# Performance work log

Measured on AMD Instinct MI355X. Metric: run time of the kernel, lower is better.

## Reference

```python
import jax, jax.numpy as jnp
import numpy as np

BN_EPS = 1e-5
TEMPERATURE = 256 ** 0.5  # sqrt(c2), since cv3 = ScaledDotProductAttention(c2)


def conv_bn_silu(x, w, gamma, beta, mean, var):
    # Conv2d(k=3, s=1, pad='same', bias=False) -> BatchNorm2d (running stats) -> SiLU
    y = jax.lax.conv_general_dilated(
        x, w, window_strides=(1, 1), padding='SAME',
        dimension_numbers=('NCHW', 'OIHW', 'NCHW'))
    scale = (gamma / jnp.sqrt(var + BN_EPS))[None, :, None, None]
    shift = (beta - mean * gamma / jnp.sqrt(var + BN_EPS))[None, :, None, None]
    y = y * scale + shift
    return y * jax.nn.sigmoid(y)  # SiLU


def setup_inputs() -> dict:
    key = jax.random.key(0)
    ks = jax.random.split(key, 8)
    B, C, H, W = 16, 256, 64, 64
    Ch = 128  # hidden channels c_ = int(c2 * e)
    x = jax.random.normal(ks[0], (B, C, H, W), dtype=jnp.float32)
    w1 = jax.random.normal(ks[1], (Ch, C, 3, 3), dtype=jnp.float32) * 0.05
    g1 = jnp.ones((Ch,), jnp.float32) + 0.1 * jax.random.normal(ks[2], (Ch,), dtype=jnp.float32)
    b1 = 0.1 * jax.random.normal(ks[3], (Ch,), dtype=jnp.float32)
    m1 = 0.1 * jax.random.normal(ks[4], (Ch,), dtype=jnp.float32)
    v1 = jnp.ones((Ch,), jnp.float32) + 0.5 * jax.random.uniform(ks[5], (Ch,), dtype=jnp.float32)
    w2 = jax.random.normal(ks[6], (C, Ch, 3, 3), dtype=jnp.float32) * 0.05
    g2 = jnp.ones((C,), jnp.float32)
    b2 = jnp.zeros((C,), jnp.float32)
    m2 = 0.1 * jax.random.normal(ks[7], (C,), dtype=jnp.float32)
    v2 = jnp.ones((C,), jnp.float32) + 0.5 * jax.random.uniform(jax.random.fold_in(key, 99), (C,), dtype=jnp.float32)
    return {"x": x, "w1": w1, "g1": g1, "b1": b1, "m1": m1, "v1": v1,
            "w2": w2, "g2": g2, "b2": b2, "m2": m2, "v2": v2}


def reference(x, w1, g1, b1, m1, v1, w2, g2, b2, m2, v2):
    y = conv_bn_silu(x, w1, g1, b1, m1, v1)       # [B, 128, H, W]
    y = conv_bn_silu(y, w2, g2, b2, m2, v2)       # [B, 256, H, W]
    B, C, H, W = y.shape
    q = y.reshape(B, C, H * W)                    # q = k^T = v, all views of y
    # channel-channel attention: scores [B, C, C]
    scores = jnp.einsum('bcn,bdn->bcd', q / TEMPERATURE, q)
    attn = jax.nn.softmax(scores, axis=-1)        # dropout is identity in eval
    out = jnp.einsum('bcd,bdn->bcn', attn, q).reshape(B, C, H, W)
    return x + out  # shortcut: c1 == c2
```

## Files before the change

kernel.cpp:

```cpp
#include <hip/hip_runtime.h>
#include <math.h>

#define BB 16
#define C1 256
#define CHD 128
#define NN 4096
#define INV_T (1.0f/16.0f)

typedef _Float16 half8 __attribute__((ext_vector_type(8)));
typedef __attribute__((ext_vector_type(4))) float f32x4;

__device__ inline unsigned short f2h(float f) {
    _Float16 h = (_Float16)f;
    return __builtin_bit_cast(unsigned short, h);
}

#define GLDS(g, l) __builtin_amdgcn_global_load_lds(                              \
    (const __attribute__((address_space(1))) unsigned int*)(g),                   \
    (__attribute__((address_space(3))) unsigned int*)(l), 16, 0, 0)

__global__ __launch_bounds__(256) void nchw_to_nhwc_f16(
    const float* __restrict__ x, unsigned short* __restrict__ xh, int C)
{
    const int c0 = blockIdx.x * 64;
    const int hp = blockIdx.y;
    const int b  = blockIdx.z;

    if (hp == 0 || hp == 65) {
        for (int idx = threadIdx.x; idx < 1024; idx += 256) {
            int w = idx >> 4, cq = (idx & 15) * 4;
            ushort4 z; z.x = z.y = z.z = z.w = 0;
            *(ushort4*)&xh[(((size_t)b * 66 + hp) * 64 + w) * C + c0 + cq] = z;
        }
        return;
    }
    const int h = hp - 1;
    __shared__ float ts[64][65];
    for (int idx = threadIdx.x; idx < 4096; idx += 256) {
        int cl = idx >> 6, w = idx & 63;
        ts[cl][w] = x[(((size_t)b * C + c0 + cl) * 64 + h) * 64 + w];
    }
    __syncthreads();
    for (int idx = threadIdx.x; idx < 1024; idx += 256) {
        int w = idx >> 4, cq = (idx & 15) * 4;
        ushort4 o;
        o.x = f2h(ts[cq + 0][w]); o.y = f2h(ts[cq + 1][w]);
        o.z = f2h(ts[cq + 2][w]); o.w = f2h(ts[cq + 3][w]);
        *(ushort4*)&xh[(((size_t)b * 66 + hp) * 64 + w) * C + c0 + cq] = o;
    }
}

__global__ __launch_bounds__(256) void pack_w_kernel(
    const float* __restrict__ w, unsigned short* __restrict__ wT, int Cout, int Cin)
{
    int idx = blockIdx.x * 256 + threadIdx.x;
    int total = Cout * Cin * 9;
    if (idx >= total) return;
    int ci = idx % Cin; int t = idx / Cin; int co = t % Cout; int kk = t / Cout;
    wT[idx] = f2h(w[((size_t)co * Cin + ci) * 9 + kk]);
}

__global__ __launch_bounds__(256) void zero_y1h_pads(unsigned short* __restrict__ y1h)
{
    int idx = blockIdx.x * 256 + threadIdx.x;
    int b = idx >> 12;
    int row = ((idx >> 11) & 1) ? 65 : 0;
    int inner = idx & 2047;
    ushort4 z; z.x = z.y = z.z = z.w = 0;
    *(ushort4*)&y1h[(((size_t)b * 66 + row) * 64) * 128 + inner * 4] = z;
}

__global__ __launch_bounds__(256) void conv_mfma_kernel(
    const unsigned short* __restrict__ xh, const unsigned short* __restrict__ wT,
    const float* __restrict__ gamma, const float* __restrict__ beta,
    const float* __restrict__ mean, const float* __restrict__ var,
    unsigned short* __restrict__ outNHWC,
    unsigned short* __restrict__ yhi, unsigned short* __restrict__ yhiT,
    int Cin, int Cout)
{
    const int tid  = threadIdx.x;
    const int wid  = tid >> 6;
    const int lane = tid & 63;
    const int ln   = lane & 15;
    const int q    = lane >> 4;
    const int coBase = blockIdx.x * 64;
    const int h0     = blockIdx.y * 4;
    const int b      = blockIdx.z;

    __shared__ unsigned short xs[6 * 66 * 32];
    __shared__ unsigned short ws[9 * 64 * 32];
    __shared__ float bnsc[64], bnsh[64];

    if (tid < 64) {
        int co = coBase + tid;
        float sc = gamma[co] * rsqrtf(var[co] + 1e-5f);
        bnsc[tid] = sc;
        bnsh[tid] = beta[co] - mean[co] * sc;
    }
    if (tid < 48) {
        int r = tid >> 3, cpart = tid & 7;
        int col = (cpart < 4) ? 0 : 65;
        ushort4 z; z.x = z.y = z.z = z.w = 0;
        *(ushort4*)&xs[r * 2112 + col * 32 + (cpart & 3) * 8] = z;
        *(ushort4*)&xs[r * 2112 + col * 32 + (cpart & 3) * 8 + 4] = z;
    }
    __syncthreads();

    f32x4 acc[4][4] = {};

    const int nChunk = Cin >> 5;
    for (int ck = 0; ck < nChunk; ck++) {
        const int ci0 = ck << 5;
        for (int it = wid; it < 60; it += 4) {
            if (it < 36) {
                int el   = it * 512 + lane * 8;
                int kkco = el >> 5;
                int kk   = kkco >> 6;
                int co   = kkco & 63;
                int cip  = el & 31;
                const unsigned short* g =
                    wT + (((size_t)kk * Cout + coBase + co) * Cin + ci0 + cip);
                GLDS(g, ws + it * 512);
            } else {
                int j = it - 36;
                int r = j >> 2, p = j & 3;
                int w   = p * 16 + (lane >> 2);
                int cip = (lane & 3) * 8;
                const unsigned short* g =
                    xh + ((((size_t)b * 66 + h0 + r) * 64 + w) * Cin + ci0 + cip);
                GLDS(g, xs + r * 2112 + (1 + p * 16) * 32);
            }
        }
        __syncthreads();

#pragma unroll
        for (int kk = 0; kk < 9; kk++) {
            const int kh = kk / 3, kw = kk % 3;
            half8 af[4], bfr[4];
#pragma unroll
            for (int mi = 0; mi < 4; mi++)
                af[mi] = *(const half8*)&ws[(kk * 64 + mi * 16 + ln) * 32 + q * 8];
#pragma unroll
            for (int ni = 0; ni < 4; ni++)
                bfr[ni] = *(const half8*)&xs[(wid + kh) * 2112 + (ni * 16 + ln + kw) * 32 + q * 8];
#pragma unroll
            for (int mi = 0; mi < 4; mi++)
#pragma unroll
                for (int ni = 0; ni < 4; ni++)
                    acc[mi][ni] = __builtin_amdgcn_mfma_f32_16x16x32_f16(
                        af[mi], bfr[ni], acc[mi][ni], 0, 0, 0);
        }
        __syncthreads();
    }

    const int orow = h0 + wid;
    if (outNHWC) {
#pragma unroll
        for (int mi = 0; mi < 4; mi++) {
            int col0 = mi * 16 + q * 4;
            float s0 = bnsc[col0 + 0], h0s = bnsh[col0 + 0];
            float s1 = bnsc[col0 + 1], h1s = bnsh[col0 + 1];
            float s2 = bnsc[col0 + 2], h2s = bnsh[col0 + 2];
            float s3 = bnsc[col0 + 3], h3s = bnsh[col0 + 3];
#pragma unroll
            for (int ni = 0; ni < 4; ni++) {
                int w = ni * 16 + ln;
                f32x4 a = acc[mi][ni];
                float t0 = a.x * s0 + h0s, t1 = a.y * s1 + h1s;
                float t2 = a.z * s2 + h2s, t3 = a.w * s3 + h3s;
                ushort4 o;
                o.x = f2h(t0 / (1.f + __expf(-t0)));
                o.y = f2h(t1 / (1.f + __expf(-t1)));
                o.z = f2h(t2 / (1.f + __expf(-t2)));
                o.w = f2h(t3 / (1.f + __expf(-t3)));
                *(ushort4*)&outNHWC[(((size_t)b * 66 + orow + 1) * 64 + w) * Cout
                                    + coBase + col0] = o;
            }
        }
    } else {
#pragma unroll
        for (int mi = 0; mi < 4; mi++) {
            int col0 = mi * 16 + q * 4;
#pragma unroll
            for (int ni = 0; ni < 4; ni++) {
                int w = ni * 16 + ln;
                f32x4 a = acc[mi][ni];
                float vals[4] = {a.x, a.y, a.z, a.w};
                ushort4 hv;
                unsigned short* hvp = (unsigned short*)&hv;
#pragma unroll
                for (int r = 0; r < 4; r++) {
                    int co = coBase + col0 + r;
                    float t = vals[r] * bnsc[col0 + r] + bnsh[col0 + r];
                    float s = t / (1.f + __expf(-t));
                    hvp[r] = f2h(s);
                    yhi[(((size_t)b * Cout + co) * 64 + orow) * 64 + w] = hvp[r];
                }
                *(ushort4*)&yhiT[((size_t)b * 4096 + orow * 64 + w) * Cout
                                 + coBase + col0] = hv;
            }
        }
    }
}

__global__ __launch_bounds__(256) void scores_mfma_kernel(
    const unsigned short* __restrict__ yhi, float* __restrict__ scores)
{
    static const int TI[10] = {0,0,0,0,1,1,1,2,2,3};
    static const int TJ[10] = {0,1,2,3,1,2,3,2,3,3};
    const int b  = blockIdx.z;
    const int ti = TI[blockIdx.x], tj = TJ[blockIdx.x];
    const int cB = ti * 64;
    const int dB = tj * 64;
    const int tid  = threadIdx.x;
    const int wid  = tid >> 6;
    const int lane = tid & 63;
    const int ln   = lane & 15;
    const int q    = lane >> 4;
    const int wm   = wid >> 1, wn = wid & 1;

    __shared__ unsigned short As[64 * 128];
    __shared__ unsigned short Bs[64 * 128];

    const int rl = lane >> 4;
    const int gl = lane & 15;

    f32x4 acc[2][2] = {};

    for (int ck = 0; ck < 32; ck++) {
        const int n0 = ck * 128;
        for (int it = wid; it < 32; it += 4) {
            const int tile = it >> 4;
            const int j = it & 15;
            const int r = j * 4 + rl;
            const int gq = gl ^ (r & 7);
            const int rowAbs = (tile ? dB : cB) + r;
            const unsigned short* g =
                yhi + ((size_t)b * 256 + rowAbs) * 4096 + n0 + gq * 8;
            GLDS(g, (tile ? Bs : As) + j * 512);
        }
        __syncthreads();

#pragma unroll
        for (int kwin = 0; kwin < 4; kwin++) {
            half8 ah[2], bh[2];
#pragma unroll
            for (int mi = 0; mi < 2; mi++) {
                int row = wm * 32 + mi * 16 + ln;
                ah[mi] = *(const half8*)&As[row * 128 + ((kwin * 4 + q) ^ (ln & 7)) * 8];
            }
#pragma unroll
            for (int ni = 0; ni < 2; ni++) {
                int row = wn * 32 + ni * 16 + ln;
                bh[ni] = *(const half8*)&Bs[row * 128 + ((kwin * 4 + q) ^ (ln & 7)) * 8];
            }
#pragma unroll
            for (int mi = 0; mi < 2; mi++)
#pragma unroll
                for (int ni = 0; ni < 2; ni++)
                    acc[mi][ni] = __builtin_amdgcn_mfma_f32_16x16x32_f16(
                        ah[mi], bh[ni], acc[mi][ni], 0, 0, 0);
        }
        __syncthreads();
    }

#pragma unroll
    for (int mi = 0; mi < 2; mi++)
#pragma unroll
        for (int ni = 0; ni < 2; ni++) {
            f32x4 a = acc[mi][ni];
            float vals[4];
            vals[0] = a.x * INV_T; vals[1] = a.y * INV_T;
            vals[2] = a.z * INV_T; vals[3] = a.w * INV_T;
            int c0 = cB + wm * 32 + mi * 16 + q * 4;
            int d  = dB + wn * 32 + ni * 16 + ln;
#pragma unroll
            for (int r = 0; r < 4; r++)
                scores[((size_t)b * C1 + c0 + r) * C1 + d] = vals[r];
            if (ti != tj) {
                float4 tv = {vals[0], vals[1], vals[2], vals[3]};
                *(float4*)&scores[((size_t)b * C1 + d) * C1 + c0] = tv;
            }
        }
}

__global__ __launch_bounds__(64) void softmax_kernel(
    const float* __restrict__ scores, unsigned short* __restrict__ attn16)
{
    const int row = blockIdx.x;
    const float* p = scores + (size_t)row * C1;
    const int lane = threadIdx.x;

    float4 v = ((const float4*)p)[lane];
    float m = fmaxf(fmaxf(v.x, v.y), fmaxf(v.z, v.w));
#pragma unroll
    for (int off = 32; off >= 1; off >>= 1)
        m = fmaxf(m, __shfl_xor(m, off, 64));

    float4 e;
    e.x = expf(v.x - m); e.y = expf(v.y - m);
    e.z = expf(v.z - m); e.w = expf(v.w - m);
    float s = e.x + e.y + e.z + e.w;
#pragma unroll
    for (int off = 32; off >= 1; off >>= 1)
        s += __shfl_xor(s, off, 64);
    float inv = 1.f / s;
    ushort4 o;
    o.x = f2h(e.x * inv); o.y = f2h(e.y * inv);
    o.z = f2h(e.z * inv); o.w = f2h(e.w * inv);
    *(ushort4*)&attn16[(size_t)row * C1 + lane * 4] = o;
}

__global__ __launch_bounds__(256) void out_mfma_kernel(
    const unsigned short* __restrict__ attn16, const unsigned short* __restrict__ yhiT,
    const float* __restrict__ x, float* __restrict__ out)
{
    const int b  = blockIdx.z;
    const int cB = blockIdx.y * 64;
    const int nB = blockIdx.x * 128;
    const int tid  = threadIdx.x;
    const int wid  = tid >> 6;
    const int lane = tid & 63;
    const int ln   = lane & 15;
    const int q    = lane >> 4;
    const int wm   = wid >> 1, wn = wid & 1;

    __shared__ unsigned short As[64 * 64];
    __shared__ unsigned short Bs[128 * 64];

    const int r8 = lane >> 3;
    const int gq = (lane & 7) ^ r8;

    f32x4 acc[2][4] = {};

    for (int ck = 0; ck < 4; ck++) {
        const int d0 = ck * 64;
        for (int it = wid; it < 24; it += 4) {
            if (it < 8) {
                const unsigned short* g =
                    attn16 + ((size_t)b * 256 + cB + it * 8 + r8) * 256 + d0 + gq * 8;
                GLDS(g, As + it * 512);
            } else {
                int j = it - 8;
                const unsigned short* g =
                    yhiT + ((size_t)b * 4096 + nB + j * 8 + r8) * 256 + d0 + gq * 8;
                GLDS(g, Bs + j * 512);
            }
        }
        __syncthreads();

#pragma unroll
        for (int kwin = 0; kwin < 2; kwin++) {
            const int cc = (((kwin * 4 + q) ^ (ln & 7))) * 8;
            half8 af[2], bfr[4];
#pragma unroll
            for (int mi = 0; mi < 2; mi++)
                af[mi] = *(const half8*)&As[(wm * 32 + mi * 16 + ln) * 64 + cc];
#pragma unroll
            for (int ni = 0; ni < 4; ni++)
                bfr[ni] = *(const half8*)&Bs[(wn * 64 + ni * 16 + ln) * 64 + cc];
#pragma unroll
            for (int mi = 0; mi < 2; mi++)
#pragma unroll
                for (int ni = 0; ni < 4; ni++)
                    acc[mi][ni] = __builtin_amdgcn_mfma_f32_16x16x32_f16(
                        af[mi], bfr[ni], acc[mi][ni], 0, 0, 0);
        }
        __syncthreads();
    }

#pragma unroll
    for (int mi = 0; mi < 2; mi++)
#pragma unroll
        for (int ni = 0; ni < 4; ni++) {
            f32x4 a = acc[mi][ni];
            float vals[4] = {a.x, a.y, a.z, a.w};
#pragma unroll
            for (int r = 0; r < 4; r++) {
                int c = cB + wm * 32 + mi * 16 + q * 4 + r;
                int n = nB + wn * 64 + ni * 16 + ln;
                size_t o = ((size_t)b * C1 + c) * NN + n;
                out[o] = x[o] + vals[r];
            }
        }
}

extern "C" void kernel_launch(void* const* d_in, const int* in_sizes, int n_in,
                              void* d_out, int out_size, void* d_ws, size_t ws_size,
                              hipStream_t stream)
{
    const float* x  = (const float*)d_in[0];
    const float* w1 = (const float*)d_in[1];
    const float* g1 = (const float*)d_in[2];
    const float* b1 = (const float*)d_in[3];
    const float* m1 = (const float*)d_in[4];
    const float* v1 = (const float*)d_in[5];
    const float* w2 = (const float*)d_in[6];
    const float* g2 = (const float*)d_in[7];
    const float* b2 = (const float*)d_in[8];
    const float* m2 = (const float*)d_in[9];
    const float* v2 = (const float*)d_in[10];
    float* out = (float*)d_out;

    unsigned short* xh   = (unsigned short*)d_ws;
    unsigned short* y1h  = xh  + (size_t)17301504;
    unsigned short* wt1  = y1h + (size_t)8650752;
    unsigned short* wt2  = wt1 + (size_t)294912;
    unsigned short* yhiT = wt2 + (size_t)294912;
    unsigned short* yhi  = xh;
    float*          sc   = (float*)y1h;
    unsigned short* attn16 = (unsigned short*)(sc + 1048576);

    nchw_to_nhwc_f16<<<dim3(C1 / 64, 66, BB), 256, 0, stream>>>(x, xh, C1);
    pack_w_kernel<<<(9 * CHD * C1 + 255) / 256, 256, 0, stream>>>(w1, wt1, CHD, C1);
    pack_w_kernel<<<(9 * C1 * CHD + 255) / 256, 256, 0, stream>>>(w2, wt2, C1, CHD);
    zero_y1h_pads<<<256, 256, 0, stream>>>(y1h);

    conv_mfma_kernel<<<dim3(CHD / 64, 16, BB), 256, 0, stream>>>(
        xh, wt1, g1, b1, m1, v1, y1h, nullptr, nullptr, C1, CHD);
    conv_mfma_kernel<<<dim3(C1 / 64, 16, BB), 256, 0, stream>>>(
        y1h, wt2, g2, b2, m2, v2, nullptr, yhi, yhiT, CHD, C1);

    scores_mfma_kernel<<<dim3(10, 1, BB), 256, 0, stream>>>(yhi, sc);
    softmax_kernel<<<dim3(BB * C1), 64, 0, stream>>>(sc, attn16);
    out_mfma_kernel<<<dim3(NN / 128, 4, BB), 256, 0, stream>>>(attn16, yhiT, x, out);
}
```

Before: 324.4 us.

## Double-buffer conv LDS staging, switch to 32x32 MFMA, 8-row 512-thread blocks

Restructures the implicit-GEMM convolution kernel so each block covers 8 output rows with 8 waves. The input-channel chunk is cut to 16 and the staging buffers are double-buffered, so the next chunk's global-to-LDS loads are issued while the current chunk is computed. The inner product moves from 16x16x32 to 32x32x16 MFMA, which cuts fragment loads per MFMA, and the epilogue is rewritten to match the new accumulator layout. The costs are smaller chunks and more barriers per chunk, a larger LDS footprint, and a reliance on async LDS loads overlapping without an explicit wait before the barrier.

New measurement: 343.7 us. +6.0%, slower.

```diff
diff --git a/kernel.cpp b/kernel.cpp
--- a/kernel.cpp
+++ b/kernel.cpp
@@ -9,6 +9,7 @@
 
 typedef _Float16 half8 __attribute__((ext_vector_type(8)));
 typedef __attribute__((ext_vector_type(4))) float f32x4;
+typedef __attribute__((ext_vector_type(16))) float f32x16;
 
 __device__ inline unsigned short f2h(float f) {
     _Float16 h = (_Float16)f;
@@ -70,7 +71,7 @@
     *(ushort4*)&y1h[(((size_t)b * 66 + row) * 64) * 128 + inner * 4] = z;
 }
 
-__global__ __launch_bounds__(256) void conv_mfma_kernel(
+__global__ __launch_bounds__(512, 4) void conv_mfma_kernel(
     const unsigned short* __restrict__ xh, const unsigned short* __restrict__ wT,
     const float* __restrict__ gamma, const float* __restrict__ beta,
     const float* __restrict__ mean, const float* __restrict__ var,
@@ -81,14 +82,14 @@
     const int tid  = threadIdx.x;
     const int wid  = tid >> 6;
     const int lane = tid & 63;
-    const int ln   = lane & 15;
-    const int q    = lane >> 4;
+    const int l31  = lane & 31;
+    const int hi   = lane >> 5;
     const int coBase = blockIdx.x * 64;
-    const int h0     = blockIdx.y * 4;
+    const int h0     = blockIdx.y * 8;
     const int b      = blockIdx.z;
 
-    __shared__ unsigned short xs[6 * 66 * 32];
-    __shared__ unsigned short ws[9 * 64 * 32];
+    __shared__ unsigned short xs[2][10560];
+    __shared__ unsigned short ws[2][9216];
     __shared__ float bnsc[64], bnsh[64];
 
     if (tid < 64) {
@@ -97,109 +98,111 @@
         bnsc[tid] = sc;
         bnsh[tid] = beta[co] - mean[co] * sc;
     }
-    if (tid < 48) {
-        int r = tid >> 3, cpart = tid & 7;
-        int col = (cpart < 4) ? 0 : 65;
+    if (tid < 160) {
+        int r    = tid >> 4;
+        int rem  = tid & 15;
+        int buf  = rem >> 3;
+        int rem2 = rem & 7;
+        int col  = (rem2 >> 2) ? 65 : 0;
+        int part = rem2 & 3;
         ushort4 z; z.x = z.y = z.z = z.w = 0;
-        *(ushort4*)&xs[r * 2112 + col * 32 + (cpart & 3) * 8] = z;
-        *(ushort4*)&xs[r * 2112 + col * 32 + (cpart & 3) * 8 + 4] = z;
-    }
+        *(ushort4*)&xs[buf][(r * 66 + col) * 16 + part * 4] = z;
+    }
+
+    auto stage = [&](int sel, int ck) {
+        const int ci0 = ck << 4;
+        for (int it = wid; it < 38; it += 8) {
+            if (it < 18) {
+                int row = it * 32 + (lane >> 1);
+                int kk  = row >> 6;
+                int co  = row & 63;
+                const unsigned short* g =
+                    wT + (((size_t)kk * Cout + coBase + co) * Cin + ci0 + (lane & 1) * 8);
+                GLDS(g, &ws[sel][it * 512]);
+            } else {
+                int j  = it - 18;
+                int r  = j >> 1;
+                int hf = j & 1;
+                int colL = hf * 32 + (lane >> 1);
+                const unsigned short* g =
+                    xh + ((((size_t)b * 66 + h0 + r) * 64 + colL) * Cin + ci0 + (lane & 1) * 8);
+                GLDS(g, &xs[sel][(r * 66 + 1 + hf * 32) * 16]);
+            }
+        }
+    };
+
+    stage(0, 0);
     __syncthreads();
 
-    f32x4 acc[4][4] = {};
-
-    const int nChunk = Cin >> 5;
-    for (int ck = 0; ck < nChunk; ck++) {
-        const int ci0 = ck << 5;
-        for (int it = wid; it < 60; it += 4) {
-            if (it < 36) {
-                int el   = it * 512 + lane * 8;
-                int kkco = el >> 5;
-                int kk   = kkco >> 6;
-                int co   = kkco & 63;
-                int cip  = el & 31;
-                const unsigned short* g =
-                    wT + (((size_t)kk * Cout + coBase + co) * Cin + ci0 + cip);
-                GLDS(g, ws + it * 512);
-            } else {
-                int j = it - 36;
-                int r = j >> 2, p = j & 3;
-                int w   = p * 16 + (lane >> 2);
-                int cip = (lane & 3) * 8;
-                const unsigned short* g =
-                    xh + ((((size_t)b * 66 + h0 + r) * 64 + w) * Cin + ci0 + cip);
-                GLDS(g, xs + r * 2112 + (1 + p * 16) * 32);
-            }
-        }
-        __syncthreads();
-
+    f32x16 acc[2][2] = {};
+
+    const int nCk = Cin >> 4;
+    int sel = 0;
+    for (int ck = 0; ck < nCk; ck++) {
+        if (ck + 1 < nCk) stage(sel ^ 1, ck + 1);
+
+        const unsigned short* wsb = &ws[sel][0];
+        const unsigned short* xsb = &xs[sel][0];
 #pragma unroll
         for (int kk = 0; kk < 9; kk++) {
             const int kh = kk / 3, kw = kk % 3;
-            half8 af[4], bfr[4];
-#pragma unroll
-            for (int mi = 0; mi < 4; mi++)
-                af[mi] = *(const half8*)&ws[(kk * 64 + mi * 16 + ln) * 32 + q * 8];
-#pragma unroll
-            for (int ni = 0; ni < 4; ni++)
-                bfr[ni] = *(const half8*)&xs[(wid + kh) * 2112 + (ni * 16 + ln + kw) * 32 + q * 8];
-#pragma unroll
-            for (int mi = 0; mi < 4; mi++)
-#pragma unroll
-                for (int ni = 0; ni < 4; ni++)
-                    acc[mi][ni] = __builtin_amdgcn_mfma_f32_16x16x32_f16(
-                        af[mi], bfr[ni], acc[mi][ni], 0, 0, 0);
+            half8 a0 = *(const half8*)&wsb[(kk * 64 +      l31) * 16 + hi * 8];
+            half8 a1 = *(const half8*)&wsb[(kk * 64 + 32 + l31) * 16 + hi * 8];
+            const unsigned short* xr = &xsb[((wid + kh) * 66 + l31 + kw) * 16 + hi * 8];
+            half8 b0 = *(const half8*)xr;
+            half8 b1 = *(const half8*)&xr[32 * 16];
+            acc[0][0] = __builtin_amdgcn_mfma_f32_32x32x16_f16(a0, b0, acc[0][0], 0, 0, 0);
+            acc[0][1] = __builtin_amdgcn_mfma_f32_32x32x16_f16(a0, b1, acc[0][1], 0, 0, 0);
+            acc[1][0] = __builtin_amdgcn_mfma_f32_32x32x16_f16(a1, b0, acc[1][0], 0, 0, 0);
+            acc[1][1] = __builtin_amdgcn_mfma_f32_32x32x16_f16(a1, b1, acc[1][1], 0, 0, 0);
         }
         __syncthreads();
+        sel ^= 1;
     }
 
     const int orow = h0 + wid;
     if (outNHWC) {
 #pragma unroll
-        for (int mi = 0; mi < 4; mi++) {
-            int col0 = mi * 16 + q * 4;
-            float s0 = bnsc[col0 + 0], h0s = bnsh[col0 + 0];
-            float s1 = bnsc[col0 + 1], h1s = bnsh[col0 + 1];
-            float s2 = bnsc[col0 + 2], h2s = bnsh[col0 + 2];
-            float s3 = bnsc[col0 + 3], h3s = bnsh[col0 + 3];
-#pragma unroll
-            for (int ni = 0; ni < 4; ni++) {
-                int w = ni * 16 + ln;
-                f32x4 a = acc[mi][ni];
-                float t0 = a.x * s0 + h0s, t1 = a.y * s1 + h1s;
-                float t2 = a.z * s2 + h2s, t3 = a.w * s3 + h3s;
-                ushort4 o;
-                o.x = f2h(t0 / (1.f + __expf(-t0)));
-                o.y = f2h(t1 / (1.f + __expf(-t1)));
-                o.z = f2h(t2 / (1.f + __expf(-t2)));
-                o.w = f2h(t3 / (1.f + __expf(-t3)));
-                *(ushort4*)&outNHWC[(((size_t)b * 66 + orow + 1) * 64 + w) * Cout
-                                    + coBase + col0] = o;
-            }
-        }
+        for (int mi = 0; mi < 2; mi++)
+#pragma unroll
+            for (int ni = 0; ni < 2; ni++) {
+                f32x16 a = acc[mi][ni];
+                int w = ni * 32 + l31;
+                size_t rowbase = (((size_t)b * 66 + orow + 1) * 64 + w) * Cout + coBase;
+#pragma unroll
+                for (int rq = 0; rq < 4; rq++) {
+                    int c0 = mi * 32 + rq * 8 + hi * 4;
+                    ushort4 o; unsigned short* op = (unsigned short*)&o;
+#pragma unroll
+                    for (int r = 0; r < 4; r++) {
+                        float t = a[rq * 4 + r] * bnsc[c0 + r] + bnsh[c0 + r];
+                        op[r] = f2h(t / (1.f + __expf(-t)));
+                    }
+                    *(ushort4*)&outNHWC[rowbase + c0] = o;
+                }
+            }
     } else {
 #pragma unroll
-        for (int mi = 0; mi < 4; mi++) {
-            int col0 = mi * 16 + q * 4;
-#pragma unroll
-            for (int ni = 0; ni < 4; ni++) {
-                int w = ni * 16 + ln;
-                f32x4 a = acc[mi][ni];
-                float vals[4] = {a.x, a.y, a.z, a.w};
-                ushort4 hv;
-                unsigned short* hvp = (unsigned short*)&hv;
-#pragma unroll
-                for (int r = 0; r < 4; r++) {
-                    int co = coBase + col0 + r;
-                    float t = vals[r] * bnsc[col0 + r] + bnsh[col0 + r];
-                    float s = t / (1.f + __expf(-t));
-                    hvp[r] = f2h(s);
-                    yhi[(((size_t)b * Cout + co) * 64 + orow) * 64 + w] = hvp[r];
+        for (int mi = 0; mi < 2; mi++)
+#pragma unroll
+            for (int ni = 0; ni < 2; ni++) {
+                f32x16 a = acc[mi][ni];
+                int w = ni * 32 + l31;
+#pragma unroll
+                for (int rq = 0; rq < 4; rq++) {
+                    int c0 = mi * 32 + rq * 8 + hi * 4;
+                    ushort4 o; unsigned short* op = (unsigned short*)&o;
+#pragma unroll
+                    for (int r = 0; r < 4; r++) {
+                        float t = a[rq * 4 + r] * bnsc[c0 + r] + bnsh[c0 + r];
+                        float s = t / (1.f + __expf(-t));
+                        op[r] = f2h(s);
+                        yhi[(((size_t)b * Cout + coBase + c0 + r) * 64 + orow) * 64 + w] = op[r];
+                    }
+                    *(ushort4*)&yhiT[((size_t)b * 4096 + (size_t)orow * 64 + w) * Cout
+                                     + coBase + c0] = o;
                 }
-                *(ushort4*)&yhiT[((size_t)b * 4096 + orow * 64 + w) * Cout
-                                 + coBase + col0] = hv;
-            }
-        }
+            }
     }
 }
 
@@ -416,9 +419,9 @@
     pack_w_kernel<<<(9 * C1 * CHD + 255) / 256, 256, 0, stream>>>(w2, wt2, C1, CHD);
     zero_y1h_pads<<<256, 256, 0, stream>>>(y1h);
 
-    conv_mfma_kernel<<<dim3(CHD / 64, 16, BB), 256, 0, stream>>>(
+    conv_mfma_kernel<<<dim3(CHD / 64, 8, BB), 512, 0, stream>>>(
         xh, wt1, g1, b1, m1, v1, y1h, nullptr, nullptr, C1, CHD);
-    conv_mfma_kernel<<<dim3(C1 / 64, 16, BB), 256, 0, stream>>>(
+    conv_mfma_kernel<<<dim3(C1 / 64, 8, BB), 512, 0, stream>>>(
         y1h, wt2, g2, b2, m2, v2, nullptr, yhi, yhiT, CHD, C1);
 
     scores_mfma_kernel<<<dim3(10, 1, BB), 256, 0, stream>>>(yhi, sc);
```
